# Optimization experiments

Hardware: AMD Instinct MI355X
Metric: run time of the kernel (lower is better)

The kernel has to match this reference:

```python
import jax, jax.numpy as jnp
import numpy as np

SOBEL_X = jnp.array([[-1., 0., 1.], [-2., 0., 2.], [-1., 0., 1.]], dtype=jnp.float32).reshape(1, 1, 3, 3)
SOBEL_Y = jnp.array([[-1., -2., -1.], [0., 0., 0.], [1., 2., 1.]], dtype=jnp.float32).reshape(1, 1, 3, 3)


def _gray(x):
    # x: (B, 3, H, W) -> (B, 1, H, W)
    if x.shape[1] == 3:
        return 0.299 * x[:, 0:1] + 0.587 * x[:, 1:2] + 0.114 * x[:, 2:3]
    return x


def _edges(g):
    # g: (B, 1, H, W); 3x3 Sobel convs with padding 1 (cross-correlation, like torch conv2d)
    dn = ('NCHW', 'OIHW', 'NCHW')
    ex = jax.lax.conv_general_dilated(g, SOBEL_X, (1, 1), ((1, 1), (1, 1)), dimension_numbers=dn)
    ey = jax.lax.conv_general_dilated(g, SOBEL_Y, (1, 1), ((1, 1), (1, 1)), dimension_numbers=dn)
    return jnp.sqrt(ex * ex + ey * ey)


def setup_inputs() -> dict:
    key = jax.random.key(0)
    k1, k2 = jax.random.split(key)
    pred = jax.random.normal(k1, (32, 3, 512, 512), dtype=jnp.float32)
    target = jax.random.normal(k2, (32, 3, 512, 512), dtype=jnp.float32)
    return {"pred": pred, "target": target}


def reference(pred, target):
    pred_edges = _edges(_gray(pred))
    target_edges = _edges(_gray(target))
    return jnp.mean(jnp.abs(pred_edges - target_edges))
```

## Files before the change

### kernel.cpp

```cpp
#include <hip/hip_runtime.h>


#define BATCH 32
#define HH 512
#define WW 512
#define TX 64
#define TY 32
#define LDS_W 72
#define LDS_W4 18
#define LDS_ROWS 34
#define SLOTS (LDS_ROWS * LDS_W4)

__global__ void zero_out_kernel(float* out) { out[0] = 0.0f; }

__global__ __launch_bounds__(256) void edge_loss_kernel(
    const float* __restrict__ pred,
    const float* __restrict__ target,
    float* __restrict__ out)
{
    __shared__ float gp[LDS_ROWS * LDS_W];
    __shared__ float gt[LDS_ROWS * LDS_W];

    const int tid = threadIdx.x;
    const int x0 = blockIdx.x * TX;
    const int y0 = blockIdx.y * TY;
    const int b  = blockIdx.z;

    const size_t img = (size_t)HH * WW;
    const float* pbase = pred   + (size_t)b * 3 * img;
    const float* tbase = target + (size_t)b * 3 * img;

    float4* gp4 = (float4*)gp;
    float4* gt4 = (float4*)gt;

    #pragma unroll
    for (int t = 0; t < 3; ++t) {
        const int i = tid + t * 256;
        if (i < SLOTS) {
            const int row = i / LDS_W4;
            const int c   = i - row * LDS_W4;
            const int gy = y0 - 1 + row;
            const int gx = x0 - 4 + 4 * c;
            float4 vp = make_float4(0.f, 0.f, 0.f, 0.f);
            float4 vt = make_float4(0.f, 0.f, 0.f, 0.f);
            if (gy >= 0 && gy < HH && gx >= 0 && gx <= WW - 4) {
                const size_t o = (size_t)gy * WW + gx;
                const float4 pr = *(const float4*)(pbase + o);
                const float4 pg = *(const float4*)(pbase + o + img);
                const float4 pb = *(const float4*)(pbase + o + 2 * img);
                const float4 tr = *(const float4*)(tbase + o);
                const float4 tg = *(const float4*)(tbase + o + img);
                const float4 tb = *(const float4*)(tbase + o + 2 * img);
                vp.x = 0.299f * pr.x + 0.587f * pg.x + 0.114f * pb.x;
                vp.y = 0.299f * pr.y + 0.587f * pg.y + 0.114f * pb.y;
                vp.z = 0.299f * pr.z + 0.587f * pg.z + 0.114f * pb.z;
                vp.w = 0.299f * pr.w + 0.587f * pg.w + 0.114f * pb.w;
                vt.x = 0.299f * tr.x + 0.587f * tg.x + 0.114f * tb.x;
                vt.y = 0.299f * tr.y + 0.587f * tg.y + 0.114f * tb.y;
                vt.z = 0.299f * tr.z + 0.587f * tg.z + 0.114f * tb.z;
                vt.w = 0.299f * tr.w + 0.587f * tg.w + 0.114f * tb.w;
            }
            gp4[i] = vp;
            gt4[i] = vt;
        }
    }
    __syncthreads();

    const int tx = tid & 63;
    const int ty = tid >> 6;
    float lsum = 0.0f;

    #pragma unroll
    for (int i = 0; i < TY / 4; ++i) {
        const int ry = ty + 4 * i;
        const float* cp = &gp[ry * LDS_W + tx + 3];
        const float* ct = &gt[ry * LDS_W + tx + 3];

        float p00 = cp[0],         p01 = cp[1],             p02 = cp[2];
        float p10 = cp[LDS_W],                              p12 = cp[LDS_W + 2];
        float p20 = cp[2*LDS_W],   p21 = cp[2*LDS_W + 1],   p22 = cp[2*LDS_W + 2];
        float ex = (p02 - p00) + 2.0f * (p12 - p10) + (p22 - p20);
        float ey = (p20 - p00) + 2.0f * (p21 - p01) + (p22 - p02);
        float ep = sqrtf(ex * ex + ey * ey);

        float t00 = ct[0],         t01 = ct[1],             t02 = ct[2];
        float t10 = ct[LDS_W],                              t12 = ct[LDS_W + 2];
        float t20 = ct[2*LDS_W],   t21 = ct[2*LDS_W + 1],   t22 = ct[2*LDS_W + 2];
        float fx = (t02 - t00) + 2.0f * (t12 - t10) + (t22 - t20);
        float fy = (t20 - t00) + 2.0f * (t21 - t01) + (t22 - t02);
        float et = sqrtf(fx * fx + fy * fy);

        lsum += fabsf(ep - et);
    }

    #pragma unroll
    for (int off = 32; off > 0; off >>= 1)
        lsum += __shfl_down(lsum, off, 64);

    __shared__ float wsum[4];
    if ((tid & 63) == 0) wsum[ty] = lsum;
    __syncthreads();
    if (tid == 0) {
        const float s = wsum[0] + wsum[1] + wsum[2] + wsum[3];
        const float inv_n = 1.0f / ((float)BATCH * HH * WW);
        atomicAdd(out, s * inv_n);
    }
}

extern "C" void kernel_launch(void* const* d_in, const int* in_sizes, int n_in,
                              void* d_out, int out_size, void* d_ws, size_t ws_size,
                              hipStream_t stream) {
    const float* pred   = (const float*)d_in[0];
    const float* target = (const float*)d_in[1];
    float* out = (float*)d_out;

    zero_out_kernel<<<1, 1, 0, stream>>>(out);

    dim3 grid(WW / TX, HH / TY, BATCH);
    edge_loss_kernel<<<grid, 256, 0, stream>>>(pred, target, out);
}
```

Before: 224.7 us.

## Split into fp16 grayscale pre-pass and a row-per-wave Sobel kernel

When the workspace is large enough, a streaming kernel first converts pred and target to fp16 grayscale images, with many independent float4 loads per thread. A second kernel then computes the Sobel magnitudes row by row, using half8 vector loads of neighbouring rows, with no LDS tiling or halo staging. The aim is to raise memory-level parallelism over the original fused tiled kernel and to halve the traffic for the intermediate image. The cost is an extra intermediate write and read plus one more launch, and fp16 rounding of the grayscale values may change the loss slightly. The old fused kernel is kept as a fallback when the workspace is too small.

After: 272.4 us. +21.2%, slower.

```diff
diff --git a/kernel.cpp b/kernel.cpp
--- a/kernel.cpp
+++ b/kernel.cpp
@@ -1,9 +1,140 @@
 #include <hip/hip_runtime.h>
 
+
+typedef _Float16 half8 __attribute__((ext_vector_type(8)));
+typedef _Float16 half4 __attribute__((ext_vector_type(4)));
 
 #define BATCH 32
 #define HH 512
 #define WW 512
+#define PLANE (HH * WW)
+#define IMGPX ((size_t)BATCH * PLANE)
+#define GRAY_BYTES (2 * IMGPX * sizeof(_Float16))
+
+__global__ void zero_out_kernel(float* out) { out[0] = 0.0f; }
+
+
+struct RGB { float4 r, g, b; };
+
+__device__ __forceinline__ RGB load_rgb(const float* __restrict__ base, unsigned u) {
+    const unsigned bb  = u >> 16;
+    const unsigned off = (u & 65535u) * 4u;
+    const float* p = base + (size_t)bb * (3 * PLANE) + off;
+    RGB x;
+    x.r = *(const float4*)p;
+    x.g = *(const float4*)(p + PLANE);
+    x.b = *(const float4*)(p + 2 * PLANE);
+    return x;
+}
+
+__device__ __forceinline__ half4 to_gray(const RGB& c) {
+    half4 h;
+    h[0] = (_Float16)(0.299f * c.r.x + 0.587f * c.g.x + 0.114f * c.b.x);
+    h[1] = (_Float16)(0.299f * c.r.y + 0.587f * c.g.y + 0.114f * c.b.y);
+    h[2] = (_Float16)(0.299f * c.r.z + 0.587f * c.g.z + 0.114f * c.b.z);
+    h[3] = (_Float16)(0.299f * c.r.w + 0.587f * c.g.w + 0.114f * c.b.w);
+    return h;
+}
+
+__global__ __launch_bounds__(256) void gray_kernel(
+    const float* __restrict__ pred,
+    const float* __restrict__ target,
+    _Float16* __restrict__ gray)
+{
+    const unsigned tid = blockIdx.x * 256u + threadIdx.x;
+    const unsigned S   = 1048576u;
+    const unsigned u0 = tid, u1 = tid + S;
+
+    RGB a = load_rgb(pred,   u0);
+    RGB b = load_rgb(pred,   u1);
+    RGB c = load_rgb(target, u0);
+    RGB d = load_rgb(target, u1);
+
+    _Float16* gp = gray;
+    _Float16* gt = gray + IMGPX;
+    *(half4*)(gp + (size_t)u0 * 4) = to_gray(a);
+    *(half4*)(gp + (size_t)u1 * 4) = to_gray(b);
+    *(half4*)(gt + (size_t)u0 * 4) = to_gray(c);
+    *(half4*)(gt + (size_t)u1 * 4) = to_gray(d);
+}
+
+
+__device__ __forceinline__ void sobel_rows(
+    const _Float16* __restrict__ row,
+    int x0, int xl, int xr, bool okm, bool okp, bool okL, bool okR,
+    float ep[8])
+{
+    const _Float16* rm = okm ? row - WW : row;
+    const _Float16* rp = okp ? row + WW : row;
+    const half8 z8 = {(_Float16)0, (_Float16)0, (_Float16)0, (_Float16)0,
+                      (_Float16)0, (_Float16)0, (_Float16)0, (_Float16)0};
+
+    const half8 mC = okm ? *(const half8*)(rm + x0) : z8;
+    const half8 mL = okm ? *(const half8*)(rm + xl) : z8;
+    const half8 mR = okm ? *(const half8*)(rm + xr) : z8;
+    const half8 cC = *(const half8*)(row + x0);
+    const half8 cL = *(const half8*)(row + xl);
+    const half8 cR = *(const half8*)(row + xr);
+    const half8 pC = okp ? *(const half8*)(rp + x0) : z8;
+    const half8 pL = okp ? *(const half8*)(rp + xl) : z8;
+    const half8 pR = okp ? *(const half8*)(rp + xr) : z8;
+
+    auto col = [&](const half8& L, const half8& C, const half8& R, int k) -> float {
+        if (k < 0) return okL ? (float)L[7] : 0.0f;
+        if (k > 7) return okR ? (float)R[0] : 0.0f;
+        return (float)C[k];
+    };
+
+    #pragma unroll
+    for (int j = 0; j < 8; ++j) {
+        const float m0 = col(mL, mC, mR, j - 1), m1 = col(mL, mC, mR, j), m2 = col(mL, mC, mR, j + 1);
+        const float c0 = col(cL, cC, cR, j - 1),                          c2 = col(cL, cC, cR, j + 1);
+        const float q0 = col(pL, pC, pR, j - 1), q1 = col(pL, pC, pR, j), q2 = col(pL, pC, pR, j + 1);
+        const float ex = (m2 - m0) + 2.0f * (c2 - c0) + (q2 - q0);
+        const float ey = (q0 + 2.0f * q1 + q2) - (m0 + 2.0f * m1 + m2);
+        ep[j] = sqrtf(ex * ex + ey * ey);
+    }
+}
+
+__global__ __launch_bounds__(256) void sobel_kernel(
+    const _Float16* __restrict__ gray, float* __restrict__ out)
+{
+    const int t    = threadIdx.x;
+    const int lane = t & 63;
+    const int wrow = blockIdx.x * 4 + (t >> 6);
+    const int y    = wrow & (HH - 1);
+
+    const _Float16* gp = gray + (size_t)wrow * WW;
+    const _Float16* gt = gp + IMGPX;
+
+    const int x0 = lane * 8;
+    const bool okm = (y > 0), okp = (y < HH - 1);
+    const bool okL = (lane > 0), okR = (lane < 63);
+    const int xl = okL ? x0 - 8 : 0;
+    const int xr = okR ? x0 + 8 : x0;
+
+    float ep[8], et[8];
+    sobel_rows(gp, x0, xl, xr, okm, okp, okL, okR, ep);
+    sobel_rows(gt, x0, xl, xr, okm, okp, okL, okR, et);
+
+    float acc = 0.0f;
+    #pragma unroll
+    for (int j = 0; j < 8; ++j) acc += fabsf(ep[j] - et[j]);
+
+    #pragma unroll
+    for (int off = 32; off > 0; off >>= 1)
+        acc += __shfl_down(acc, off, 64);
+
+    __shared__ float wsum[4];
+    if (lane == 0) wsum[t >> 6] = acc;
+    __syncthreads();
+    if (t == 0) {
+        const float s = wsum[0] + wsum[1] + wsum[2] + wsum[3];
+        atomicAdd(out, s * (1.0f / (float)IMGPX));
+    }
+}
+
+
 #define TX 64
 #define TY 32
 #define LDS_W 72
@@ -11,31 +142,25 @@
 #define LDS_ROWS 34
 #define SLOTS (LDS_ROWS * LDS_W4)
 
-__global__ void zero_out_kernel(float* out) { out[0] = 0.0f; }
-
-__global__ __launch_bounds__(256) void edge_loss_kernel(
+__global__ __launch_bounds__(256) void fused_kernel(
     const float* __restrict__ pred,
     const float* __restrict__ target,
     float* __restrict__ out)
 {
     __shared__ float gp[LDS_ROWS * LDS_W];
     __shared__ float gt[LDS_ROWS * LDS_W];
-
     const int tid = threadIdx.x;
     const int x0 = blockIdx.x * TX;
     const int y0 = blockIdx.y * TY;
     const int b  = blockIdx.z;
-
     const size_t img = (size_t)HH * WW;
     const float* pbase = pred   + (size_t)b * 3 * img;
     const float* tbase = target + (size_t)b * 3 * img;
-
     float4* gp4 = (float4*)gp;
     float4* gt4 = (float4*)gt;
-
-    #pragma unroll
-    for (int t = 0; t < 3; ++t) {
-        const int i = tid + t * 256;
+    #pragma unroll
+    for (int tt = 0; tt < 3; ++tt) {
+        const int i = tid + tt * 256;
         if (i < SLOTS) {
             const int row = i / LDS_W4;
             const int c   = i - row * LDS_W4;
@@ -51,61 +176,54 @@
                 const float4 tr = *(const float4*)(tbase + o);
                 const float4 tg = *(const float4*)(tbase + o + img);
                 const float4 tb = *(const float4*)(tbase + o + 2 * img);
-                vp.x = 0.299f * pr.x + 0.587f * pg.x + 0.114f * pb.x;
-                vp.y = 0.299f * pr.y + 0.587f * pg.y + 0.114f * pb.y;
-                vp.z = 0.299f * pr.z + 0.587f * pg.z + 0.114f * pb.z;
-                vp.w = 0.299f * pr.w + 0.587f * pg.w + 0.114f * pb.w;
-                vt.x = 0.299f * tr.x + 0.587f * tg.x + 0.114f * tb.x;
-                vt.y = 0.299f * tr.y + 0.587f * tg.y + 0.114f * tb.y;
-                vt.z = 0.299f * tr.z + 0.587f * tg.z + 0.114f * tb.z;
-                vt.w = 0.299f * tr.w + 0.587f * tg.w + 0.114f * tb.w;
+                vp.x = 0.299f*pr.x + 0.587f*pg.x + 0.114f*pb.x;
+                vp.y = 0.299f*pr.y + 0.587f*pg.y + 0.114f*pb.y;
+                vp.z = 0.299f*pr.z + 0.587f*pg.z + 0.114f*pb.z;
+                vp.w = 0.299f*pr.w + 0.587f*pg.w + 0.114f*pb.w;
+                vt.x = 0.299f*tr.x + 0.587f*tg.x + 0.114f*tb.x;
+                vt.y = 0.299f*tr.y + 0.587f*tg.y + 0.114f*tb.y;
+                vt.z = 0.299f*tr.z + 0.587f*tg.z + 0.114f*tb.z;
+                vt.w = 0.299f*tr.w + 0.587f*tg.w + 0.114f*tb.w;
             }
             gp4[i] = vp;
             gt4[i] = vt;
         }
     }
     __syncthreads();
-
     const int tx = tid & 63;
     const int ty = tid >> 6;
     float lsum = 0.0f;
-
     #pragma unroll
     for (int i = 0; i < TY / 4; ++i) {
         const int ry = ty + 4 * i;
         const float* cp = &gp[ry * LDS_W + tx + 3];
         const float* ct = &gt[ry * LDS_W + tx + 3];
-
-        float p00 = cp[0],         p01 = cp[1],             p02 = cp[2];
-        float p10 = cp[LDS_W],                              p12 = cp[LDS_W + 2];
-        float p20 = cp[2*LDS_W],   p21 = cp[2*LDS_W + 1],   p22 = cp[2*LDS_W + 2];
+        float p00 = cp[0],       p01 = cp[1],           p02 = cp[2];
+        float p10 = cp[LDS_W],                          p12 = cp[LDS_W + 2];
+        float p20 = cp[2*LDS_W], p21 = cp[2*LDS_W + 1], p22 = cp[2*LDS_W + 2];
         float ex = (p02 - p00) + 2.0f * (p12 - p10) + (p22 - p20);
         float ey = (p20 - p00) + 2.0f * (p21 - p01) + (p22 - p02);
-        float ep = sqrtf(ex * ex + ey * ey);
-
-        float t00 = ct[0],         t01 = ct[1],             t02 = ct[2];
-        float t10 = ct[LDS_W],                              t12 = ct[LDS_W + 2];
-        float t20 = ct[2*LDS_W],   t21 = ct[2*LDS_W + 1],   t22 = ct[2*LDS_W + 2];
+        float epv = sqrtf(ex * ex + ey * ey);
+        float t00 = ct[0],       t01 = ct[1],           t02 = ct[2];
+        float t10 = ct[LDS_W],                          t12 = ct[LDS_W + 2];
+        float t20 = ct[2*LDS_W], t21 = ct[2*LDS_W + 1], t22 = ct[2*LDS_W + 2];
         float fx = (t02 - t00) + 2.0f * (t12 - t10) + (t22 - t20);
         float fy = (t20 - t00) + 2.0f * (t21 - t01) + (t22 - t02);
-        float et = sqrtf(fx * fx + fy * fy);
-
-        lsum += fabsf(ep - et);
-    }
-
+        float etv = sqrtf(fx * fx + fy * fy);
+        lsum += fabsf(epv - etv);
+    }
     #pragma unroll
     for (int off = 32; off > 0; off >>= 1)
         lsum += __shfl_down(lsum, off, 64);
-
     __shared__ float wsum[4];
     if ((tid & 63) == 0) wsum[ty] = lsum;
     __syncthreads();
     if (tid == 0) {
         const float s = wsum[0] + wsum[1] + wsum[2] + wsum[3];
-        const float inv_n = 1.0f / ((float)BATCH * HH * WW);
-        atomicAdd(out, s * inv_n);
-    }
-}
+        atomicAdd(out, s * (1.0f / (float)IMGPX));
+    }
+}
+
 
 extern "C" void kernel_launch(void* const* d_in, const int* in_sizes, int n_in,
                               void* d_out, int out_size, void* d_ws, size_t ws_size,
@@ -116,6 +234,12 @@
 
     zero_out_kernel<<<1, 1, 0, stream>>>(out);
 
-    dim3 grid(WW / TX, HH / TY, BATCH);
-    edge_loss_kernel<<<grid, 256, 0, stream>>>(pred, target, out);
-}
+    if (ws_size >= GRAY_BYTES) {
+        _Float16* gray = (_Float16*)d_ws;
+        gray_kernel<<<4096, 256, 0, stream>>>(pred, target, gray);
+        sobel_kernel<<<4096, 256, 0, stream>>>(gray, out);
+    } else {
+        dim3 grid(WW / TX, HH / TY, BATCH);
+        fused_kernel<<<grid, 256, 0, stream>>>(pred, target, out);
+    }
+}
```
